# Kernel tuning notes

Measured on AMD Instinct MI355X. Metric: run time of the kernel, lower is better.

## Reference

```python
import jax, jax.numpy as jnp
import numpy as np

B, N, ND = 32, 512, 8        # batch, graph_size, node_dim
L, H, D = 4, 8, 512          # layers, heads, embed_dim
DK = D // H                  # key_dim = val_dim = 64
F = 2048                     # feed_forward_hidden
EPS = 1e-5


def setup_inputs() -> dict:
    key = jax.random.key(0)
    ks = jax.random.split(key, 16)
    u = lambda k, shape, s: jax.random.uniform(k, shape, jnp.float32, -s, s)
    x = jax.random.normal(ks[0], (B, N, ND), dtype=jnp.float32)
    mask = jax.random.randint(ks[1], (B, N, N), 0, 2).astype(jnp.int32)  # 1 = masked
    return {
        "x": x,
        "mask": mask,
        # init_embed Linear(node_dim, embed_dim)
        "We": u(ks[2], (ND, D), 1.0 / np.sqrt(ND)),
        "be": u(ks[3], (D,), 1.0 / np.sqrt(ND)),
        # per-head projections, stacked over layers; torch init: uniform(-1/sqrt(last_dim), ...)
        "Wq": u(ks[4], (L, H, D, DK), 1.0 / np.sqrt(DK)),
        "Wk": u(ks[5], (L, H, D, DK), 1.0 / np.sqrt(DK)),
        "Wv": u(ks[6], (L, H, D, DK), 1.0 / np.sqrt(DK)),
        "Wo": u(ks[7], (L, H, DK, D), 1.0 / np.sqrt(D)),
        # BatchNorm1d affine params (torch default: weight=1, bias=0)
        "g1": jnp.ones((L, D), jnp.float32), "bt1": jnp.zeros((L, D), jnp.float32),
        "g2": jnp.ones((L, D), jnp.float32), "bt2": jnp.zeros((L, D), jnp.float32),
        # FFN
        "W1": u(ks[8], (L, D, F), 1.0 / np.sqrt(D)),
        "bf1": u(ks[9], (L, F), 1.0 / np.sqrt(D)),
        "W2": u(ks[10], (L, F, D), 1.0 / np.sqrt(F)),
        "bf2": u(ks[11], (L, D), 1.0 / np.sqrt(F)),
    }


def _batch_norm(h, g, b):
    # BatchNorm1d in training mode over flattened (B*N, D), biased variance
    hf = h.reshape(-1, h.shape[-1])
    mu = hf.mean(axis=0)
    var = hf.var(axis=0)
    return (h - mu) * jax.lax.rsqrt(var + EPS) * g + b


def reference(x, mask, We, be, Wq, Wk, Wv, Wo, g1, bt1, W1, bf1, W2, bf2, g2, bt2):
    m = mask.astype(bool)[None]                      # [1,B,N,N], True = masked
    scale = 1.0 / np.sqrt(Wq.shape[-1])
    h = x @ We + be                                  # [B,N,D]
    for l in range(Wq.shape[0]):
        # hand-rolled per-head MHA (q = h, self-attention)
        Q = jnp.einsum('bnd,hdk->hbnk', h, Wq[l])
        K = jnp.einsum('bnd,hdk->hbnk', h, Wk[l])
        V = jnp.einsum('bnd,hdv->hbnv', h, Wv[l])
        scores = jnp.einsum('hbqk,hbnk->hbqn', Q, K) * scale   # [H,B,N,N]
        scores = jnp.where(m, -jnp.inf, scores)
        attn = jax.nn.softmax(scores, axis=-1)
        attn = jnp.where(m, 0.0, attn)               # second mask-zeroing pass
        heads = jnp.einsum('hbqn,hbnv->hbqv', attn, V)
        out = jnp.einsum('hbqv,hvd->bqd', heads, Wo[l])
        h = _batch_norm(h + out, g1[l], bt1[l])      # residual + BN
        ff = jax.nn.relu(h @ W1[l] + bf1[l]) @ W2[l] + bf2[l]
        h = _batch_norm(h + ff, g2[l], bt2[l])       # residual + BN
    return (h, h.mean(axis=1))
```

## Files before the change

kernel.cpp:

```cpp
#include <hip/hip_runtime.h>
#include <hip/hip_fp16.h>
#include <math.h>

#define BN_ROWS 16384
#define DIM 512
#define FF 2048
#define LAYERS 4
#define NSEQ 512
#define BATCH 32

typedef _Float16 f16;
typedef __attribute__((ext_vector_type(8))) _Float16 f16x8;
typedef __attribute__((ext_vector_type(4))) _Float16 f16x4;
typedef __attribute__((ext_vector_type(4))) float f32x4;
typedef unsigned long long u64;

__device__ __forceinline__ f32x4 mfma_f16(f16x8 a, f16x8 b, f32x4 c) {
    return __builtin_amdgcn_mfma_f32_16x16x32_f16(a, b, c, 0, 0, 0);
}
__device__ __forceinline__ void gload_lds16(const f16* g, f16* l) {
    __builtin_amdgcn_global_load_lds(
        (const __attribute__((address_space(1))) unsigned int*)g,
        (__attribute__((address_space(3))) unsigned int*)l, 16, 0, 0);
}

__global__ __launch_bounds__(256)
void pack_qkv(const float* __restrict__ Wq, const float* __restrict__ Wk,
              const float* __restrict__ Wv, f16* __restrict__ oh) {
    size_t i = (size_t)blockIdx.x * 256 + threadIdx.x;
    int d = i & 511;
    size_t rr = i >> 9;
    int row = (int)(rr % 1536);
    int lay = (int)(rr / 1536);
    int which = row >> 9, hh = (row >> 6) & 7, k = row & 63;
    const float* W = which == 0 ? Wq : which == 1 ? Wk : Wv;
    oh[i] = (f16)W[(((size_t)lay * 8 + hh) * 512 + d) * 64 + k];
}

__global__ __launch_bounds__(256)
void transpose_w(const float* __restrict__ in, f16* __restrict__ oh, int R, int C) {
    size_t i = (size_t)blockIdx.x * 256 + threadIdx.x;
    int r = (int)(i % R);
    size_t t = i / R;
    int c = (int)(t % C);
    int lay = (int)(t / C);
    oh[i] = (f16)in[((size_t)lay * R + r) * C + c];
}

__global__ __launch_bounds__(256)
void pack_mask(const int* __restrict__ mask, u64* __restrict__ pm) {
    int wid = (blockIdx.x * 256 + threadIdx.x) >> 6;
    int lane = threadIdx.x & 63;
    for (int i = 0; i < 64; i++) {
        size_t word = (size_t)wid * 64 + i;
        u64 bal = __ballot(mask[word * 64 + lane] != 0);
        if (lane == 0) pm[word] = bal;
    }
}

__global__ __launch_bounds__(512)
void embed_kernel(const float* __restrict__ x, const float* __restrict__ We,
                  const float* __restrict__ be, float* __restrict__ h,
                  f16* __restrict__ hf) {
    int row = blockIdx.x, d = threadIdx.x;
    const float* xr = x + (size_t)row * 8;
    float acc = be[d];
#pragma unroll
    for (int c = 0; c < 8; c++) acc += xr[c] * We[c * DIM + d];
    size_t idx = (size_t)row * DIM + d;
    h[idx] = acc;
    hf[idx] = (f16)acc;
}

template<int OUT>
__global__ __launch_bounds__(256)
void gemm_f16(const f16* __restrict__ A, const f16* __restrict__ Bt,
              const float* __restrict__ bias,
              void* __restrict__ O0, void* __restrict__ O1, void* __restrict__ O2,
              int M, int N, int K) {
    __shared__ f16 As[2][4096];
    __shared__ f16 Bs[2][4096];
    const int gx = gridDim.x;
    const int nwg = gx * gridDim.y;
    const int id = blockIdx.y * gx + blockIdx.x;
    const int chunk = nwg >> 3;
    const int sid = (id & 7) * chunk + (id >> 3);
    const int row0 = (sid / gx) * 128, col0 = (sid % gx) * 128;

    const int tid = threadIdx.x, l = tid & 63, w = tid >> 6;
    const int wr = w >> 1, wc = w & 1;
    const int fr = l & 15, fq = l >> 4;
    const int srow = l >> 2, skg = (l & 3) * 8;

    f32x4 acc[4][4] = {};
    const f16* Ab = A + (size_t)(row0 + w * 32 + srow) * K + skg;
    const f16* Bb = Bt + (size_t)(col0 + w * 32 + srow) * K + skg;
    const size_t a16 = (size_t)16 * K;
    const int nt = K >> 5;

    gload_lds16(Ab,       &As[0][(w * 2 + 0) * 512]);
    gload_lds16(Ab + a16, &As[0][(w * 2 + 1) * 512]);
    gload_lds16(Bb,       &Bs[0][(w * 2 + 0) * 512]);
    gload_lds16(Bb + a16, &Bs[0][(w * 2 + 1) * 512]);

    for (int kt = 0; kt < nt; kt++) {
        const int buf = kt & 1;
        __syncthreads();
        if (kt + 1 < nt) {
            const int k0 = (kt + 1) * 32;
            gload_lds16(Ab + k0,       &As[buf ^ 1][(w * 2 + 0) * 512]);
            gload_lds16(Ab + a16 + k0, &As[buf ^ 1][(w * 2 + 1) * 512]);
            gload_lds16(Bb + k0,       &Bs[buf ^ 1][(w * 2 + 0) * 512]);
            gload_lds16(Bb + a16 + k0, &Bs[buf ^ 1][(w * 2 + 1) * 512]);
        }
        f16x8 a[4], b[4];
#pragma unroll
        for (int i = 0; i < 4; i++)
            a[i] = *(const f16x8*)&As[buf][(wr * 64 + i * 16 + fr) * 32 + fq * 8];
#pragma unroll
        for (int j = 0; j < 4; j++)
            b[j] = *(const f16x8*)&Bs[buf][(wc * 64 + j * 16 + fr) * 32 + fq * 8];
#pragma unroll
        for (int i = 0; i < 4; i++)
#pragma unroll
            for (int j = 0; j < 4; j++)
                acc[i][j] = mfma_f16(a[i], b[j], acc[i][j]);
    }

    if (OUT == 1) {
        f16* C = (f16*)O0;
#pragma unroll
        for (int j = 0; j < 4; j++) {
            int gcol = col0 + wc * 64 + j * 16 + fr;
            float bv = bias[gcol];
#pragma unroll
            for (int i = 0; i < 4; i++) {
                int gr = row0 + wr * 64 + i * 16 + fq * 4;
#pragma unroll
                for (int r = 0; r < 4; r++)
                    C[(size_t)(gr + r) * N + gcol] = (f16)fmaxf(acc[i][j][r] + bv, 0.f);
            }
        }
    } else if (OUT == 2) {
        f16* Qo = (f16*)O0; f16* Ko = (f16*)O1; f16* Vo = (f16*)O2;
#pragma unroll
        for (int j = 0; j < 4; j++) {
            int gcol = col0 + wc * 64 + j * 16 + fr;
            if (gcol < 1024) {
                f16* dst = gcol < 512 ? Qo : Ko;
                int cc = gcol & 511;
#pragma unroll
                for (int i = 0; i < 4; i++) {
                    int gr = row0 + wr * 64 + i * 16 + fq * 4;
#pragma unroll
                    for (int r = 0; r < 4; r++)
                        dst[(size_t)(gr + r) * 512 + cc] = (f16)acc[i][j][r];
                }
            } else {
                int hh = (gcol - 1024) >> 6, v = gcol & 63;
#pragma unroll
                for (int i = 0; i < 4; i++) {
                    int gr = row0 + wr * 64 + i * 16 + fq * 4;
                    int b = gr >> 9, n = gr & 511;
                    f16x4 sv;
#pragma unroll
                    for (int r = 0; r < 4; r++) sv[r] = (f16)acc[i][j][r];
                    *(f16x4*)&Vo[(((size_t)b * 8 + hh) * 64 + v) * 512 + n] = sv;
                }
            }
        }
    } else {
        float* hres = (float*)O0;
        float* st   = (float*)O1;
#pragma unroll
        for (int j = 0; j < 4; j++) {
            int gcol = col0 + wc * 64 + j * 16 + fr;
            float bv = bias ? bias[gcol] : 0.f;
            float csum = 0.f, csq = 0.f;
#pragma unroll
            for (int i = 0; i < 4; i++) {
                int gr = row0 + wr * 64 + i * 16 + fq * 4;
#pragma unroll
                for (int r = 0; r < 4; r++) {
                    size_t idx = (size_t)(gr + r) * N + gcol;
                    float v = acc[i][j][r] + bv + hres[idx];
                    hres[idx] = v;
                    csum += v; csq += v * v;
                }
            }
            csum += __shfl_down(csum, 32, 64); csum += __shfl_down(csum, 16, 64);
            csq  += __shfl_down(csq,  32, 64); csq  += __shfl_down(csq,  16, 64);
            if (fq == 0) {
                atomicAdd(&st[gcol], csum);
                atomicAdd(&st[gcol + 512], csq);
            }
        }
    }
}

__global__ __launch_bounds__(256)
void attn_flash(const f16* __restrict__ Q, const f16* __restrict__ Kg,
                const f16* __restrict__ Vt, const u64* __restrict__ pmask,
                f16* __restrict__ attf) {
    int id = blockIdx.x;
    int wgid = (id & 7) * 128 + (id >> 3);
    int qc = wgid & 3;
    int gid = wgid >> 2;
    int b = gid & 31, hd = gid >> 5;

    __shared__ f16 Kl[2][4096];
    __shared__ f16 Vl[2][4096];
    __shared__ f16 Plds[4][1024];

    const int tid = threadIdx.x, w = tid >> 6, l = tid & 63;
    const int fr = l & 15, fq = l >> 4;

    const int brow = qc * 128 + w * 32;
    const size_t qbase = ((size_t)b * NSEQ + brow) * DIM + hd * 64;
    f16x8 qa[2][2];
#pragma unroll
    for (int sub = 0; sub < 2; sub++)
#pragma unroll
        for (int ks = 0; ks < 2; ks++)
            qa[sub][ks] = *(const f16x8*)(Q + qbase + (size_t)(sub * 16 + fr) * DIM + ks * 32 + fq * 8);

    const f16* ksrc = Kg + (size_t)b * NSEQ * DIM + hd * 64;
    const f16* vsrc = Vt + ((size_t)b * 8 + hd) * 64 * 512;
    const u64* mrow = pmask + ((size_t)b * NSEQ + brow) * 8;

    const int sr = tid & 63;
    const int sg0 = tid >> 6;
    const int sg1 = sg0 + 4;

    const float SC = 0.18033688011112042f;
    const float THR = 11.0f;

    float mu[2][4];
    f32x4 O[2][4] = {};
    f32x4 S1[2] = {};
#pragma unroll
    for (int s = 0; s < 2; s++)
#pragma unroll
        for (int r = 0; r < 4; r++) mu[s][r] = -1e30f;

    f16x8 vones;
#pragma unroll
    for (int i = 0; i < 8; i++) vones[i] = (f16)1.0f;

    char* Pb = (char*)&Plds[w][0];

    gload_lds16(ksrc + (size_t)sr * DIM + sg0 * 8, &Kl[0][tid * 8]);
    gload_lds16(ksrc + (size_t)sr * DIM + sg1 * 8, &Kl[0][2048 + tid * 8]);
    gload_lds16(vsrc + (size_t)sr * 512 + sg0 * 8, &Vl[0][tid * 8]);
    gload_lds16(vsrc + (size_t)sr * 512 + sg1 * 8, &Vl[0][2048 + tid * 8]);

    for (int c = 0; c < 8; c++) {
        const int buf = c & 1;
        __syncthreads();
        if (c < 7) {
            const int n1 = (c + 1) * 64;
            gload_lds16(ksrc + (size_t)(n1 + sr) * DIM + sg0 * 8, &Kl[buf ^ 1][tid * 8]);
            gload_lds16(ksrc + (size_t)(n1 + sr) * DIM + sg1 * 8, &Kl[buf ^ 1][2048 + tid * 8]);
            gload_lds16(vsrc + (size_t)sr * 512 + n1 + sg0 * 8,   &Vl[buf ^ 1][tid * 8]);
            gload_lds16(vsrc + (size_t)sr * 512 + n1 + sg1 * 8,   &Vl[buf ^ 1][2048 + tid * 8]);
        }

        f16x8 kb[4][2];
#pragma unroll
        for (int nt = 0; nt < 4; nt++)
#pragma unroll
            for (int ks = 0; ks < 2; ks++)
                kb[nt][ks] = *(const f16x8*)&Kl[buf][(ks * 4 + fq) * 512 + (nt * 16 + fr) * 8];

        f32x4 ps[2][4];
#pragma unroll
        for (int sub = 0; sub < 2; sub++)
#pragma unroll
            for (int nt = 0; nt < 4; nt++) {
                f32x4 a = {};
                a = mfma_f16(qa[sub][0], kb[nt][0], a);
                a = mfma_f16(qa[sub][1], kb[nt][1], a);
                ps[sub][nt] = a;
            }
#pragma unroll
        for (int sub = 0; sub < 2; sub++)
#pragma unroll
            for (int rr = 0; rr < 4; rr++) {
                u64 bits = mrow[(size_t)(sub * 16 + fq * 4 + rr) * 8 + c];
#pragma unroll
                for (int nt = 0; nt < 4; nt++) {
                    float u = ps[sub][nt][rr] * SC;
                    ps[sub][nt][rr] = ((bits >> (nt * 16 + fr)) & 1ull) ? -INFINITY : u;
                }
            }

        f16x8 vb[4][2];
#pragma unroll
        for (int vt = 0; vt < 4; vt++)
#pragma unroll
            for (int ks = 0; ks < 2; ks++)
                vb[vt][ks] = *(const f16x8*)&Vl[buf][(ks * 4 + fq) * 512 + (vt * 16 + fr) * 8];

#pragma unroll
        for (int sub = 0; sub < 2; sub++) {
            float lmax[4];
#pragma unroll
            for (int rr = 0; rr < 4; rr++)
                lmax[rr] = fmaxf(fmaxf(ps[sub][0][rr], ps[sub][1][rr]),
                                 fmaxf(ps[sub][2][rr], ps[sub][3][rr]));
            bool over = (lmax[0] > mu[sub][0] + THR) | (lmax[1] > mu[sub][1] + THR) |
                        (lmax[2] > mu[sub][2] + THR) | (lmax[3] > mu[sub][3] + THR);
            if (__any(over)) {
#pragma unroll
                for (int rr = 0; rr < 4; rr++) {
                    float v = lmax[rr];
#pragma unroll
                    for (int msk = 1; msk < 16; msk <<= 1)
                        v = fmaxf(v, __shfl_xor(v, msk, 64));
                    float mn = fmaxf(mu[sub][rr], v);
                    float sc = exp2f(mu[sub][rr] - mn);
                    mu[sub][rr] = mn;
                    S1[sub][rr] *= sc;
#pragma unroll
                    for (int vt = 0; vt < 4; vt++)
                        O[sub][vt][rr] *= sc;
                }
            }
#pragma unroll
            for (int nt = 0; nt < 4; nt++)
#pragma unroll
                for (int rr = 0; rr < 4; rr++)
                    ps[sub][nt][rr] = exp2f(ps[sub][nt][rr] - mu[sub][rr]);
#pragma unroll
            for (int nt = 0; nt < 4; nt++)
#pragma unroll
                for (int rr = 0; rr < 4; rr++) {
                    int row = fq * 4 + rr;
                    int byte = ((row * 64 + nt * 16 + fr) * 2) ^ ((row & 7) << 4);
                    *(f16*)(Pb + byte) = (f16)ps[sub][nt][rr];
                }
            f16x8 pa[2];
#pragma unroll
            for (int ks = 0; ks < 2; ks++) {
                int byte = ((fr * 64 + ks * 32 + fq * 8) * 2) ^ ((fr & 7) << 4);
                pa[ks] = *(const f16x8*)(Pb + byte);
            }
            S1[sub] = mfma_f16(pa[0], vones, S1[sub]);
            S1[sub] = mfma_f16(pa[1], vones, S1[sub]);
#pragma unroll
            for (int vt = 0; vt < 4; vt++) {
                O[sub][vt] = mfma_f16(pa[0], vb[vt][0], O[sub][vt]);
                O[sub][vt] = mfma_f16(pa[1], vb[vt][1], O[sub][vt]);
            }
        }
    }
#pragma unroll
    for (int sub = 0; sub < 2; sub++) {
        float inv[4];
#pragma unroll
        for (int rr = 0; rr < 4; rr++) inv[rr] = 1.f / S1[sub][rr];
#pragma unroll
        for (int vt = 0; vt < 4; vt++)
#pragma unroll
            for (int rr = 0; rr < 4; rr++) {
                float v = O[sub][vt][rr] * inv[rr];
                size_t idx = ((size_t)b * NSEQ + brow + sub * 16 + fq * 4 + rr) * DIM
                             + hd * 64 + vt * 16 + fr;
                attf[idx] = (f16)v;
            }
    }
}

__global__ __launch_bounds__(256)
void bn_apply(float* __restrict__ h, f16* __restrict__ hf,
              const float* __restrict__ sums, const float* __restrict__ g,
              const float* __restrict__ bt, float* __restrict__ outp) {
    size_t i4 = (size_t)blockIdx.x * 256 + threadIdx.x;
    size_t idx = i4 * 4;
    int c = (int)(idx & (DIM - 1));
    float4 hv = *(float4*)&h[idx];
    float4 s4 = *(const float4*)&sums[c];
    float4 q4 = *(const float4*)&sums[DIM + c];
    float4 g4 = *(const float4*)&g[c];
    float4 b4 = *(const float4*)&bt[c];
    float o[4];
    const float invn = 1.f / BN_ROWS;
#pragma unroll
    for (int j = 0; j < 4; j++) {
        float mu = ((const float*)&s4)[j] * invn;
        float var = ((const float*)&q4)[j] * invn - mu * mu;
        o[j] = (((const float*)&hv)[j] - mu) * rsqrtf(var + 1e-5f)
               * ((const float*)&g4)[j] + ((const float*)&b4)[j];
    }
    *(float4*)&h[idx] = *(float4*)o;
    if (outp) *(float4*)&outp[idx] = *(float4*)o;
    f16x4 s;
#pragma unroll
    for (int j = 0; j < 4; j++) s[j] = (f16)o[j];
    *(f16x4*)&hf[idx] = s;
}

__global__ __launch_bounds__(512)
void mean_kernel(const float* __restrict__ src, float* __restrict__ out2) {
    int b = blockIdx.x, seg = blockIdx.y, d = threadIdx.x;
    float acc = 0.f;
    for (int n = seg * 64; n < seg * 64 + 64; n++)
        acc += src[((size_t)b * NSEQ + n) * DIM + d];
    atomicAdd(&out2[b * DIM + d], acc * (1.f / NSEQ));
}

extern "C" void kernel_launch(void* const* d_in, const int* in_sizes, int n_in,
                              void* d_out, int out_size, void* d_ws, size_t ws_size,
                              hipStream_t stream) {
    const float* x   = (const float*)d_in[0];
    const int*   mask= (const int*)d_in[1];
    const float* We  = (const float*)d_in[2];
    const float* be  = (const float*)d_in[3];
    const float* Wq  = (const float*)d_in[4];
    const float* Wk  = (const float*)d_in[5];
    const float* Wv  = (const float*)d_in[6];
    const float* Wo  = (const float*)d_in[7];
    const float* g1  = (const float*)d_in[8];
    const float* bt1 = (const float*)d_in[9];
    const float* g2  = (const float*)d_in[10];
    const float* bt2 = (const float*)d_in[11];
    const float* W1  = (const float*)d_in[12];
    const float* bf1 = (const float*)d_in[13];
    const float* W2  = (const float*)d_in[14];
    const float* bf2 = (const float*)d_in[15];
    float* out = (float*)d_out;

    const size_t MiB = 1ull << 20;
    const size_t M1 = (size_t)BN_ROWS * DIM;
    char* base = (char*)d_ws;
    float* h     = (float*)base;
    f16*   hf    = (f16*)(base + 32 * MiB);
    f16*   Qf    = (f16*)(base + 48 * MiB);
    f16*   Kf    = (f16*)(base + 64 * MiB);
    f16*   Vt    = (f16*)(base + 80 * MiB);
    f16*   attf  = (f16*)(base + 96 * MiB);
    f16*   ffh   = (f16*)(base + 48 * MiB);
    float* stats = (float*)(base + 112 * MiB);
    u64*   pmask = (u64*)(base + 112 * MiB + 65536);
    f16*   wqkv  = (f16*)(base + 114 * MiB);
    f16*   wo    = wqkv + (size_t)4 * 1536 * 512;
    f16*   w1t   = wo   + (size_t)4 * 512 * 512;
    f16*   w2t   = w1t  + (size_t)4 * 2048 * 512;

    pack_qkv<<<dim3(4 * 1536 * 512 / 256), dim3(256), 0, stream>>>(Wq, Wk, Wv, wqkv);
    transpose_w<<<dim3(4 * 512 * 512 / 256), dim3(256), 0, stream>>>(Wo, wo, 512, 512);
    transpose_w<<<dim3(4 * 512 * 2048 / 256), dim3(256), 0, stream>>>(W1, w1t, 512, 2048);
    transpose_w<<<dim3(4 * 2048 * 512 / 256), dim3(256), 0, stream>>>(W2, w2t, 2048, 512);
    pack_mask<<<dim3(512), dim3(256), 0, stream>>>(mask, pmask);
    hipMemsetAsync(out + M1, 0, BATCH * DIM * sizeof(float), stream);

    embed_kernel<<<dim3(BN_ROWS), dim3(512), 0, stream>>>(x, We, be, h, hf);

    for (int l = 0; l < LAYERS; l++) {
        gemm_f16<2><<<dim3(1536 / 128, 128), dim3(256), 0, stream>>>(
            hf, wqkv + (size_t)l * 1536 * 512, nullptr, Qf, Kf, Vt,
            BN_ROWS, 1536, 512);

        attn_flash<<<dim3(1024), dim3(256), 0, stream>>>(Qf, Kf, Vt, pmask, attf);

        hipMemsetAsync(stats, 0, 1024 * sizeof(float), stream);
        gemm_f16<3><<<dim3(512 / 128, 128), dim3(256), 0, stream>>>(
            attf, wo + (size_t)l * 512 * 512, nullptr, h, stats, nullptr,
            BN_ROWS, 512, 512);
        bn_apply<<<dim3(M1 / 1024), dim3(256), 0, stream>>>(
            h, hf, stats, g1 + l * DIM, bt1 + l * DIM, nullptr);

        hipMemsetAsync(stats, 0, 1024 * sizeof(float), stream);
        gemm_f16<1><<<dim3(FF / 128, BN_ROWS / 128), dim3(256), 0, stream>>>(
            hf, w1t + (size_t)l * FF * DIM, bf1 + (size_t)l * FF,
            ffh, nullptr, nullptr, BN_ROWS, FF, DIM);
        gemm_f16<3><<<dim3(DIM / 128, BN_ROWS / 128), dim3(256), 0, stream>>>(
            ffh, w2t + (size_t)l * DIM * FF, bf2 + (size_t)l * DIM,
            h, stats, nullptr, BN_ROWS, DIM, FF);

        float* outp = (l == LAYERS - 1) ? out : nullptr;
        bn_apply<<<dim3(M1 / 1024), dim3(256), 0, stream>>>(
            h, hf, stats, g2 + l * DIM, bt2 + l * DIM, outp);
    }

    mean_kernel<<<dim3(BATCH, 8), dim3(512), 0, stream>>>(out, out + M1);
}
```

Measured before the change: 1.224 ms.

## Store residual stream in fp16, triple-buffer GEMM with LDS swizzle, fold Q scale

The fp32 residual buffer h is removed and the single fp16 copy serves as both residual and GEMM input, so bn_apply and the residual GEMM epilogues move half the bytes. The GEMM goes from double to triple-buffered LDS staging with explicit vmcnt waits, and uses an XOR swizzle on the LDS reads to cut bank conflicts. The softmax scale is folded into the Q projection epilogue, which removes a multiply from the attention inner loop. Keeping the residual in fp16 loses precision across layers, and the swizzle on the write side relies on global_load_lds lane placement matching the read-side XOR.

```diff
diff --git a/kernel.cpp b/kernel.cpp
--- a/kernel.cpp
+++ b/kernel.cpp
@@ -60,16 +60,13 @@
 
 __global__ __launch_bounds__(512)
 void embed_kernel(const float* __restrict__ x, const float* __restrict__ We,
-                  const float* __restrict__ be, float* __restrict__ h,
-                  f16* __restrict__ hf) {
+                  const float* __restrict__ be, f16* __restrict__ h16) {
     int row = blockIdx.x, d = threadIdx.x;
     const float* xr = x + (size_t)row * 8;
     float acc = be[d];
 #pragma unroll
     for (int c = 0; c < 8; c++) acc += xr[c] * We[c * DIM + d];
-    size_t idx = (size_t)row * DIM + d;
-    h[idx] = acc;
-    hf[idx] = (f16)acc;
+    h16[(size_t)row * DIM + d] = (f16)acc;
 }
 
 template<int OUT>
@@ -78,8 +75,8 @@
               const float* __restrict__ bias,
               void* __restrict__ O0, void* __restrict__ O1, void* __restrict__ O2,
               int M, int N, int K) {
-    __shared__ f16 As[2][4096];
-    __shared__ f16 Bs[2][4096];
+    __shared__ f16 As[3][4096];
+    __shared__ f16 Bs[3][4096];
     const int gx = gridDim.x;
     const int nwg = gx * gridDim.y;
     const int id = blockIdx.y * gx + blockIdx.x;
@@ -90,7 +87,9 @@
     const int tid = threadIdx.x, l = tid & 63, w = tid >> 6;
     const int wr = w >> 1, wc = w & 1;
     const int fr = l & 15, fq = l >> 4;
-    const int srow = l >> 2, skg = (l & 3) * 8;
+    const int srow = l >> 2;
+    const int skg = ((l & 3) ^ ((l >> 3) & 3)) * 8;
+    const int fqs8 = (fq ^ ((fr >> 1) & 3)) * 8;
 
     f32x4 acc[4][4] = {};
     const f16* Ab = A + (size_t)(row0 + w * 32 + srow) * K + skg;
@@ -98,28 +97,30 @@
     const size_t a16 = (size_t)16 * K;
     const int nt = K >> 5;
 
-    gload_lds16(Ab,       &As[0][(w * 2 + 0) * 512]);
-    gload_lds16(Ab + a16, &As[0][(w * 2 + 1) * 512]);
-    gload_lds16(Bb,       &Bs[0][(w * 2 + 0) * 512]);
-    gload_lds16(Bb + a16, &Bs[0][(w * 2 + 1) * 512]);
+    auto stage = [&](int buf, int k0) {
+        gload_lds16(Ab + k0,       &As[buf][(w * 2 + 0) * 512]);
+        gload_lds16(Ab + a16 + k0, &As[buf][(w * 2 + 1) * 512]);
+        gload_lds16(Bb + k0,       &Bs[buf][(w * 2 + 0) * 512]);
+        gload_lds16(Bb + a16 + k0, &Bs[buf][(w * 2 + 1) * 512]);
+    };
+
+    stage(0, 0);
+    stage(1, 32);
 
     for (int kt = 0; kt < nt; kt++) {
-        const int buf = kt & 1;
-        __syncthreads();
-        if (kt + 1 < nt) {
-            const int k0 = (kt + 1) * 32;
-            gload_lds16(Ab + k0,       &As[buf ^ 1][(w * 2 + 0) * 512]);
-            gload_lds16(Ab + a16 + k0, &As[buf ^ 1][(w * 2 + 1) * 512]);
-            gload_lds16(Bb + k0,       &Bs[buf ^ 1][(w * 2 + 0) * 512]);
-            gload_lds16(Bb + a16 + k0, &Bs[buf ^ 1][(w * 2 + 1) * 512]);
-        }
+        const int buf = kt % 3;
+        if (kt + 1 < nt) asm volatile("s_waitcnt vmcnt(4)" ::: "memory");
+        else             asm volatile("s_waitcnt vmcnt(0)" ::: "memory");
+        __builtin_amdgcn_s_barrier();
+        __builtin_amdgcn_sched_barrier(0);
+        if (kt + 2 < nt) stage((kt + 2) % 3, (kt + 2) * 32);
         f16x8 a[4], b[4];
 #pragma unroll
         for (int i = 0; i < 4; i++)
-            a[i] = *(const f16x8*)&As[buf][(wr * 64 + i * 16 + fr) * 32 + fq * 8];
+            a[i] = *(const f16x8*)&As[buf][(wr * 64 + i * 16 + fr) * 32 + fqs8];
 #pragma unroll
         for (int j = 0; j < 4; j++)
-            b[j] = *(const f16x8*)&Bs[buf][(wc * 64 + j * 16 + fr) * 32 + fq * 8];
+            b[j] = *(const f16x8*)&Bs[buf][(wc * 64 + j * 16 + fr) * 32 + fqs8];
 #pragma unroll
         for (int i = 0; i < 4; i++)
 #pragma unroll
@@ -142,19 +143,22 @@
             }
         }
     } else if (OUT == 2) {
+        const float SCQ = 0.18033688011112042f;
         f16* Qo = (f16*)O0; f16* Ko = (f16*)O1; f16* Vo = (f16*)O2;
 #pragma unroll
         for (int j = 0; j < 4; j++) {
             int gcol = col0 + wc * 64 + j * 16 + fr;
             if (gcol < 1024) {
-                f16* dst = gcol < 512 ? Qo : Ko;
+                bool isQ = gcol < 512;
+                f16* dst = isQ ? Qo : Ko;
+                float sc = isQ ? SCQ : 1.0f;
                 int cc = gcol & 511;
 #pragma unroll
                 for (int i = 0; i < 4; i++) {
                     int gr = row0 + wr * 64 + i * 16 + fq * 4;
 #pragma unroll
                     for (int r = 0; r < 4; r++)
-                        dst[(size_t)(gr + r) * 512 + cc] = (f16)acc[i][j][r];
+                        dst[(size_t)(gr + r) * 512 + cc] = (f16)(acc[i][j][r] * sc);
                 }
             } else {
                 int hh = (gcol - 1024) >> 6, v = gcol & 63;
@@ -170,8 +174,8 @@
             }
         }
     } else {
-        float* hres = (float*)O0;
-        float* st   = (float*)O1;
+        f16* hres = (f16*)O0;
+        float* st  = (float*)O1;
 #pragma unroll
         for (int j = 0; j < 4; j++) {
             int gcol = col0 + wc * 64 + j * 16 + fr;
@@ -183,8 +187,8 @@
 #pragma unroll
                 for (int r = 0; r < 4; r++) {
                     size_t idx = (size_t)(gr + r) * N + gcol;
-                    float v = acc[i][j][r] + bv + hres[idx];
-                    hres[idx] = v;
+                    float v = acc[i][j][r] + bv + (float)hres[idx];
+                    hres[idx] = (f16)v;
                     csum += v; csq += v * v;
                 }
             }
@@ -232,7 +236,6 @@
     const int sg0 = tid >> 6;
     const int sg1 = sg0 + 4;
 
-    const float SC = 0.18033688011112042f;
     const float THR = 11.0f;
 
     float mu[2][4];
@@ -288,10 +291,8 @@
             for (int rr = 0; rr < 4; rr++) {
                 u64 bits = mrow[(size_t)(sub * 16 + fq * 4 + rr) * 8 + c];
 #pragma unroll
-                for (int nt = 0; nt < 4; nt++) {
-                    float u = ps[sub][nt][rr] * SC;
-                    ps[sub][nt][rr] = ((bits >> (nt * 16 + fr)) & 1ull) ? -INFINITY : u;
-                }
+                for (int nt = 0; nt < 4; nt++)
+                    if ((bits >> (nt * 16 + fr)) & 1ull) ps[sub][nt][rr] = -INFINITY;
             }
 
         f16x8 vb[4][2];
@@ -372,32 +373,29 @@
 }
 
 __global__ __launch_bounds__(256)
-void bn_apply(float* __restrict__ h, f16* __restrict__ hf,
-              const float* __restrict__ sums, const float* __restrict__ g,
-              const float* __restrict__ bt, float* __restrict__ outp) {
-    size_t i4 = (size_t)blockIdx.x * 256 + threadIdx.x;
-    size_t idx = i4 * 4;
+void bn_apply(f16* __restrict__ h16, const float* __restrict__ sums,
+              const float* __restrict__ g, const float* __restrict__ bt,
+              float* __restrict__ outp) {
+    size_t i8 = (size_t)blockIdx.x * 256 + threadIdx.x;
+    size_t idx = i8 * 8;
     int c = (int)(idx & (DIM - 1));
-    float4 hv = *(float4*)&h[idx];
-    float4 s4 = *(const float4*)&sums[c];
-    float4 q4 = *(const float4*)&sums[DIM + c];
-    float4 g4 = *(const float4*)&g[c];
-    float4 b4 = *(const float4*)&bt[c];
-    float o[4];
+    f16x8 hv = *(f16x8*)&h16[idx];
+    float o[8];
     const float invn = 1.f / BN_ROWS;
 #pragma unroll
-    for (int j = 0; j < 4; j++) {
-        float mu = ((const float*)&s4)[j] * invn;
-        float var = ((const float*)&q4)[j] * invn - mu * mu;
-        o[j] = (((const float*)&hv)[j] - mu) * rsqrtf(var + 1e-5f)
-               * ((const float*)&g4)[j] + ((const float*)&b4)[j];
-    }
-    *(float4*)&h[idx] = *(float4*)o;
-    if (outp) *(float4*)&outp[idx] = *(float4*)o;
-    f16x4 s;
-#pragma unroll
-    for (int j = 0; j < 4; j++) s[j] = (f16)o[j];
-    *(f16x4*)&hf[idx] = s;
+    for (int j = 0; j < 8; j++) {
+        float mu = sums[c + j] * invn;
+        float var = sums[DIM + c + j] * invn - mu * mu;
+        o[j] = ((float)hv[j] - mu) * rsqrtf(var + 1e-5f) * g[c + j] + bt[c + j];
+    }
+    f16x8 s;
+#pragma unroll
+    for (int j = 0; j < 8; j++) s[j] = (f16)o[j];
+    *(f16x8*)&h16[idx] = s;
+    if (outp) {
+        *(float4*)&outp[idx]     = (float4){o[0], o[1], o[2], o[3]};
+        *(float4*)&outp[idx + 4] = (float4){o[4], o[5], o[6], o[7]};
+    }
 }
 
 __global__ __launch_bounds__(512)
@@ -433,16 +431,15 @@
     const size_t MiB = 1ull << 20;
     const size_t M1 = (size_t)BN_ROWS * DIM;
     char* base = (char*)d_ws;
-    float* h     = (float*)base;
-    f16*   hf    = (f16*)(base + 32 * MiB);
-    f16*   Qf    = (f16*)(base + 48 * MiB);
-    f16*   Kf    = (f16*)(base + 64 * MiB);
-    f16*   Vt    = (f16*)(base + 80 * MiB);
-    f16*   attf  = (f16*)(base + 96 * MiB);
-    f16*   ffh   = (f16*)(base + 48 * MiB);
-    float* stats = (float*)(base + 112 * MiB);
-    u64*   pmask = (u64*)(base + 112 * MiB + 65536);
-    f16*   wqkv  = (f16*)(base + 114 * MiB);
+    f16*   h16   = (f16*)base;
+    f16*   Qf    = (f16*)(base + 16 * MiB);
+    f16*   Kf    = (f16*)(base + 32 * MiB);
+    f16*   Vt    = (f16*)(base + 48 * MiB);
+    f16*   attf  = (f16*)(base + 64 * MiB);
+    f16*   ffh   = (f16*)(base + 16 * MiB);
+    float* stats = (float*)(base + 80 * MiB);
+    u64*   pmask = (u64*)(base + 80 * MiB + 65536);
+    f16*   wqkv  = (f16*)(base + 82 * MiB);
     f16*   wo    = wqkv + (size_t)4 * 1536 * 512;
     f16*   w1t   = wo   + (size_t)4 * 512 * 512;
     f16*   w2t   = w1t  + (size_t)4 * 2048 * 512;
@@ -454,33 +451,33 @@
     pack_mask<<<dim3(512), dim3(256), 0, stream>>>(mask, pmask);
     hipMemsetAsync(out + M1, 0, BATCH * DIM * sizeof(float), stream);
 
-    embed_kernel<<<dim3(BN_ROWS), dim3(512), 0, stream>>>(x, We, be, h, hf);
+    embed_kernel<<<dim3(BN_ROWS), dim3(512), 0, stream>>>(x, We, be, h16);
 
     for (int l = 0; l < LAYERS; l++) {
         gemm_f16<2><<<dim3(1536 / 128, 128), dim3(256), 0, stream>>>(
-            hf, wqkv + (size_t)l * 1536 * 512, nullptr, Qf, Kf, Vt,
+            h16, wqkv + (size_t)l * 1536 * 512, nullptr, Qf, Kf, Vt,
             BN_ROWS, 1536, 512);
 
         attn_flash<<<dim3(1024), dim3(256), 0, stream>>>(Qf, Kf, Vt, pmask, attf);
 
         hipMemsetAsync(stats, 0, 1024 * sizeof(float), stream);
         gemm_f16<3><<<dim3(512 / 128, 128), dim3(256), 0, stream>>>(
-            attf, wo + (size_t)l * 512 * 512, nullptr, h, stats, nullptr,
+            attf, wo + (size_t)l * 512 * 512, nullptr, h16, stats, nullptr,
             BN_ROWS, 512, 512);
-        bn_apply<<<dim3(M1 / 1024), dim3(256), 0, stream>>>(
-            h, hf, stats, g1 + l * DIM, bt1 + l * DIM, nullptr);
+        bn_apply<<<dim3(M1 / 2048), dim3(256), 0, stream>>>(
+            h16, stats, g1 + l * DIM, bt1 + l * DIM, nullptr);
 
         hipMemsetAsync(stats, 0, 1024 * sizeof(float), stream);
         gemm_f16<1><<<dim3(FF / 128, BN_ROWS / 128), dim3(256), 0, stream>>>(
-            hf, w1t + (size_t)l * FF * DIM, bf1 + (size_t)l * FF,
+            h16, w1t + (size_t)l * FF * DIM, bf1 + (size_t)l * FF,
             ffh, nullptr, nullptr, BN_ROWS, FF, DIM);
-        gemm_f16<3><<<dim3(DIM / 128, BN_ROWS / 128), dim3(256), 0, stream>>>(
+        gemm_f16<3><<<dim3(512 / 128, 128), dim3(256), 0, stream>>>(
             ffh, w2t + (size_t)l * DIM * FF, bf2 + (size_t)l * DIM,
-            h, stats, nullptr, BN_ROWS, DIM, FF);
+            h16, stats, nullptr, BN_ROWS, 512, FF);
 
         float* outp = (l == LAYERS - 1) ? out : nullptr;
-        bn_apply<<<dim3(M1 / 1024), dim3(256), 0, stream>>>(
-            h, hf, stats, g2 + l * DIM, bt2 + l * DIM, outp);
+        bn_apply<<<dim3(M1 / 2048), dim3(256), 0, stream>>>(
+            h16, stats, g2 + l * DIM, bt2 + l * DIM, outp);
     }
 
     mean_kernel<<<dim3(BATCH, 8), dim3(512), 0, stream>>>(out, out + M1);
```

Result: faster. 1.187 ms (-3.0%).
